# Optimization experiments

Measured on AMD Instinct MI355X. Metric: run time of the kernel, lower is better.

Reference implementation:

```python
import math
import jax, jax.numpy as jnp
import numpy as np

N_HEAD = 16; HEAD_DIM = 64; CHUNK = 64; NS_STEPS = 5; OMEGA = 16; POLY_DEG = 2; KCONV = 4


def short_conv(x, w, b):
    # x: (B,T,D), causal depthwise conv per ShortConv
    B, T, D = x.shape
    xt = jnp.transpose(x, (0, 2, 1))
    xt = jnp.pad(xt, ((0, 0), (0, 0), (KCONV - 1, 0)))
    y = jax.lax.conv_general_dilated(xt, w.astype(x.dtype), window_strides=(1,), padding='VALID',
                                     dimension_numbers=('NCW', 'OIW', 'NCW'), feature_group_count=D)
    y = y + b.astype(x.dtype)[:, None]
    return jnp.transpose(y, (0, 2, 1))


def rms_norm(x):
    ms = jnp.mean(x * x, axis=-1, keepdims=True)
    return x * jax.lax.rsqrt(ms + 1e-6)


def poly_features(x):
    coeffs = [1.0 / math.factorial(i) for i in range(1, POLY_DEG + 1)]
    res = coeffs[0] * x
    xp = x
    for i in range(1, POLY_DEG):
        xp = xp * x
        res = res + coeffs[i] * xp
    return res


def polar_express(X, steps):
    # Newton-Schulz / Polar-Express orthogonalization (Muon quintic coefficients)
    a, b, c = 3.4445, -4.7750, 2.0315
    n = jnp.sqrt(jnp.sum(X * X, axis=(-2, -1), keepdims=True)) + 1e-7
    X = X / n
    for _ in range(steps):
        XXt = X @ jnp.swapaxes(X, -1, -2)
        X = a * X + (b * XXt + c * (XXt @ XXt)) @ X
    return X


def omega_aggregate(u, gamma, w):
    # sliding-window weighted sum over chunk axis (axis=1) via cumsum difference
    cs = u.shape[1]
    cum = jnp.cumsum(gamma * u, axis=1)
    if w >= cs:
        return cum
    shifted = jnp.concatenate([jnp.zeros_like(cum[:, :w]), cum[:, :-w]], axis=1)
    return cum - shifted


def linear_scan(h_init, gates, inputs):
    # h_t = gate_t * h_{t-1} + input_t via associative scan over axis=1
    extra = inputs.ndim - gates.ndim
    g = gates.reshape(gates.shape + (1,) * extra)
    first = g[:, 0:1] * h_init[:, None] + inputs[:, 0:1]
    xs = jnp.concatenate([first, inputs[:, 1:]], axis=1)
    gs = jnp.concatenate([jnp.zeros_like(g[:, 0:1]), g[:, 1:]], axis=1)

    def fn(a, b):
        ga, xa = a
        gb, xb = b
        return (ga * gb, gb * xa + xb)

    _, h_all = jax.lax.associative_scan(fn, (gs, xs), axis=1)
    return h_all, h_all[:, -1]


def atlas_forward(x, Wq, Wk, Wv, Wproj, conv_q_w, conv_q_b, conv_k_w, conv_k_b,
                  conv_v_w, conv_v_b, Wa, We, Wt, Wg):
    B, T, C = x.shape
    H, D, cs = N_HEAD, HEAD_DIM, CHUNK
    nc = T // cs
    q = rms_norm(short_conv(x @ Wq.T, conv_q_w, conv_q_b).reshape(B, T, H, D))
    k = rms_norm(short_conv(x @ Wk.T, conv_k_w, conv_k_b).reshape(B, T, H, D))
    k = poly_features(k)  # phi(k)
    v = short_conv(x @ Wv.T, conv_v_w, conv_v_b).reshape(B, T, H, D)
    alpha = jax.nn.sigmoid(x @ Wa.T)[..., None]  # (B,T,H,1)
    eta = jax.nn.sigmoid(x @ We.T)[..., None]
    theta = jax.nn.sigmoid(x @ Wt.T)[..., None]
    gamma = jax.nn.sigmoid(x @ Wg.T)[..., None]

    def chunked(a):
        a = a.reshape((B, nc, cs) + a.shape[2:])
        return jnp.moveaxis(a, 1, 0)  # (nc, B, cs, ...)

    qc, kc, vc, ac, ec, tc, gc = map(chunked, (q, k, v, alpha, eta, theta, gamma))
    M0 = jnp.zeros((B, H, D, D), x.dtype)
    S0 = jnp.zeros_like(M0)

    def body(carry, inp):
        M, S = carry
        q_c, k_c, v_c, a_c, e_c, t_c, g_c = inp
        pred = jnp.einsum('bhvk,bchk->bchv', M, k_c)
        err = pred - v_c
        u = 2.0 * jnp.einsum('bchv,bchk->bchvk', err, k_c)  # (B,cs,H,D,D)
        u = omega_aggregate(u, g_c[..., None], OMEGA)
        th = jnp.squeeze(t_c, -1)
        mom = -(e_c[..., None] * u)
        chunk_S, S = linear_scan(S, th, mom)
        chunk_S_orth = polar_express(chunk_S, NS_STEPS)
        al = jnp.squeeze(a_c, -1)
        M_all, M = linear_scan(M, al, chunk_S_orth)
        y_c = jnp.einsum('bchvk,bchk->bchv', M_all, q_c)
        return (M, S), y_c

    (_, _), ys = jax.lax.scan(body, (M0, S0), (qc, kc, vc, ac, ec, tc, gc))
    y = jnp.moveaxis(ys, 0, 1).reshape(B, T, C)
    return y @ Wproj.T


def setup_inputs() -> dict:
    key = jax.random.key(0)
    ks = jax.random.split(key, 16)
    B, T, C, H = 2, 2048, 1024, 16
    s = 0.02
    return {
        'x': jax.random.normal(ks[0], (B, T, C), jnp.float32),
        'Wq': jax.random.normal(ks[1], (C, C), jnp.float32) * s,
        'Wk': jax.random.normal(ks[2], (C, C), jnp.float32) * s,
        'Wv': jax.random.normal(ks[3], (C, C), jnp.float32) * s,
        'Wproj': jax.random.normal(ks[4], (C, C), jnp.float32) * s,
        'conv_q_w': jax.random.normal(ks[5], (C, 1, KCONV), jnp.float32) * s,
        'conv_q_b': jnp.zeros((C,), jnp.float32),
        'conv_k_w': jax.random.normal(ks[6], (C, 1, KCONV), jnp.float32) * s,
        'conv_k_b': jnp.zeros((C,), jnp.float32),
        'conv_v_w': jax.random.normal(ks[7], (C, 1, KCONV), jnp.float32) * s,
        'conv_v_b': jnp.zeros((C,), jnp.float32),
        'Wa': jax.random.normal(ks[8], (H, C), jnp.float32) * s,
        'We': jax.random.normal(ks[9], (H, C), jnp.float32) * s,
        'Wt': jax.random.normal(ks[10], (H, C), jnp.float32) * s,
        'Wg': jax.random.normal(ks[11], (H, C), jnp.float32) * s,
    }


def reference(x, Wq, Wk, Wv, Wproj, conv_q_w, conv_q_b, conv_k_w, conv_k_b,
              conv_v_w, conv_v_b, Wa, We, Wt, Wg):
    return atlas_forward(x, Wq, Wk, Wv, Wproj, conv_q_w, conv_q_b, conv_k_w, conv_k_b,
                         conv_v_w, conv_v_b, Wa, We, Wt, Wg)
```

## Files before the change

kernel.cpp:

```cpp
#include <hip/hip_runtime.h>
#include <hip/hip_bf16.h>
#include <hip/hip_fp16.h>
#include <math.h>

#define B_ 2
#define T_ 2048
#define C_ 1024
#define H_ 16
#define D_ 64
#define CS_ 64
#define NC_ 32
#define NS_ 5
#define IST2 72

typedef __attribute__((ext_vector_type(8))) _Float16 f16x8;
typedef __attribute__((ext_vector_type(4))) float f32x4;

__global__ __launch_bounds__(256) void split16_kernel(const float* __restrict__ src,
                                                      _Float16* __restrict__ dst,
                                                      int n) {
    int i = (blockIdx.x * 256 + threadIdx.x) * 8;
    if (i >= n) return;
    float4 a = *(const float4*)&src[i];
    float4 b = *(const float4*)&src[i + 4];
    union { _Float16 h[8]; uint4 u; } o;
    o.h[0] = (_Float16)a.x; o.h[1] = (_Float16)a.y;
    o.h[2] = (_Float16)a.z; o.h[3] = (_Float16)a.w;
    o.h[4] = (_Float16)b.x; o.h[5] = (_Float16)b.y;
    o.h[6] = (_Float16)b.z; o.h[7] = (_Float16)b.w;
    *(uint4*)&dst[i] = o.u;
}

__global__ __launch_bounds__(256, 1) void gemm16(const _Float16* __restrict__ A,
                                                 const _Float16* __restrict__ Bm,
                                                 float* __restrict__ out) {
    __shared__ __align__(16) _Float16 sA[128 * 72];
    __shared__ __align__(16) _Float16 sB[128 * 72];
    int tid = threadIdx.x;
    int m0 = blockIdx.y * 128, n0 = blockIdx.x * 128;
    int w = tid >> 6, lane = tid & 63, q = lane >> 4, c = lane & 15;
    int mq = (w >> 1) * 64, nq = (w & 1) * 64;
    f32x4 acc[4][4];
    #pragma unroll
    for (int i = 0; i < 4; i++)
        #pragma unroll
        for (int j = 0; j < 4; j++) acc[i][j] = (f32x4){0.f, 0.f, 0.f, 0.f};
    int lrow = tid >> 2, lseg = (tid & 3) * 16;
    for (int kt = 0; kt < C_; kt += 64) {
        #pragma unroll
        for (int rr = 0; rr < 2; rr++) {
            int row = lrow + rr * 64;
            const size_t ga = (size_t)(m0 + row) * C_ + kt + lseg;
            const size_t gb = (size_t)(n0 + row) * C_ + kt + lseg;
            f16x8 va0 = *(const f16x8*)&A[ga];
            f16x8 va1 = *(const f16x8*)&A[ga + 8];
            f16x8 vb0 = *(const f16x8*)&Bm[gb];
            f16x8 vb1 = *(const f16x8*)&Bm[gb + 8];
            *(f16x8*)&sA[row * 72 + lseg] = va0;
            *(f16x8*)&sA[row * 72 + lseg + 8] = va1;
            *(f16x8*)&sB[row * 72 + lseg] = vb0;
            *(f16x8*)&sB[row * 72 + lseg + 8] = vb1;
        }
        __syncthreads();
        #pragma unroll
        for (int t = 0; t < 2; t++) {
            f16x8 af[4], bfr[4];
            #pragma unroll
            for (int i = 0; i < 4; i++)
                af[i] = *(const f16x8*)&sA[(mq + 16 * i + c) * 72 + t * 32 + q * 8];
            #pragma unroll
            for (int j = 0; j < 4; j++)
                bfr[j] = *(const f16x8*)&sB[(nq + 16 * j + c) * 72 + t * 32 + q * 8];
            #pragma unroll
            for (int i = 0; i < 4; i++)
                #pragma unroll
                for (int j = 0; j < 4; j++)
                    acc[i][j] = __builtin_amdgcn_mfma_f32_16x16x32_f16(af[i], bfr[j], acc[i][j], 0, 0, 0);
        }
        __syncthreads();
    }
    #pragma unroll
    for (int i = 0; i < 4; i++)
        #pragma unroll
        for (int j = 0; j < 4; j++)
            #pragma unroll
            for (int r = 0; r < 4; r++)
                out[(size_t)(m0 + mq + 16 * i + 4 * q + r) * C_ + n0 + nq + 16 * j + c] = acc[i][j][r];
}

__global__ __launch_bounds__(256) void conv_kernel(const float* __restrict__ xin,
                                                   const float* __restrict__ w,
                                                   const float* __restrict__ bias,
                                                   float* __restrict__ out, int mode) {
    int bt = blockIdx.x;
    int t = bt & (T_ - 1);
    int tid = threadIdx.x;
    int c0 = tid * 4;
    float4 w4[4];
    #pragma unroll
    for (int i = 0; i < 4; i++) w4[i] = *(const float4*)&w[(c0 + i) * 4];
    float4 bi = *(const float4*)&bias[c0];
    float4 xs[4];
    #pragma unroll
    for (int j = 0; j < 4; j++) {
        int tt = t - 3 + j;
        xs[j] = (tt >= 0) ? *(const float4*)&xin[(bt - 3 + j) * C_ + c0]
                          : make_float4(0.f, 0.f, 0.f, 0.f);
    }
    float y0 = bi.x + w4[0].x * xs[0].x + w4[0].y * xs[1].x + w4[0].z * xs[2].x + w4[0].w * xs[3].x;
    float y1 = bi.y + w4[1].x * xs[0].y + w4[1].y * xs[1].y + w4[1].z * xs[2].y + w4[1].w * xs[3].y;
    float y2 = bi.z + w4[2].x * xs[0].z + w4[2].y * xs[1].z + w4[2].z * xs[2].z + w4[2].w * xs[3].z;
    float y3 = bi.w + w4[3].x * xs[0].w + w4[3].y * xs[1].w + w4[3].z * xs[2].w + w4[3].w * xs[3].w;
    if (mode >= 1) {
        float ss = y0 * y0 + y1 * y1 + y2 * y2 + y3 * y3;
        ss += __shfl_xor(ss, 1);
        ss += __shfl_xor(ss, 2);
        ss += __shfl_xor(ss, 4);
        ss += __shfl_xor(ss, 8);
        float sc = rsqrtf(ss * (1.f / 64.f) + 1e-6f);
        y0 *= sc; y1 *= sc; y2 *= sc; y3 *= sc;
        if (mode == 2) {
            y0 += 0.5f * y0 * y0; y1 += 0.5f * y1 * y1;
            y2 += 0.5f * y2 * y2; y3 += 0.5f * y3 * y3;
        }
    }
    *(float4*)&out[bt * C_ + c0] = make_float4(y0, y1, y2, y3);
}

__global__ __launch_bounds__(256) void gates_kernel(const float* __restrict__ x,
                                                    const float* __restrict__ Wa,
                                                    const float* __restrict__ We,
                                                    const float* __restrict__ Wt,
                                                    const float* __restrict__ Wg,
                                                    float* __restrict__ gates) {
    __shared__ float xs[C_];
    int bt = blockIdx.x, tid = threadIdx.x;
    *(float4*)&xs[tid * 4] = *(const float4*)&x[bt * C_ + tid * 4];
    __syncthreads();
    int dot = tid >> 2, l = tid & 3;
    int g = dot >> 4, h = dot & 15;
    const float* Wp = (g == 0) ? Wa : (g == 1) ? We : (g == 2) ? Wt : Wg;
    const float* Wr = Wp + h * C_;
    float p = 0.f;
    for (int c = l * 4; c < C_; c += 16) {
        float4 wv = *(const float4*)&Wr[c];
        float4 xv = *(const float4*)&xs[c];
        p += wv.x * xv.x + wv.y * xv.y + wv.z * xv.z + wv.w * xv.w;
    }
    p += __shfl_xor(p, 1);
    p += __shfl_xor(p, 2);
    if (l == 0) gates[g * (B_ * T_ * H_) + bt * H_ + h] = 1.f / (1.f + __expf(-p));
}

__global__ __launch_bounds__(256) void chunk_s_kernel(const float* __restrict__ kbuf,
                                                      const float* __restrict__ vbuf,
                                                      const float* __restrict__ gates,
                                                      const float* __restrict__ Mc,
                                                      float* __restrict__ Sc,
                                                      float* __restrict__ chunkS,
                                                      int chunk) {
    __shared__ float Kc[CS_][68];
    __shared__ float Mrow[8][68];
    __shared__ float errS[CS_][8];
    __shared__ float thS[CS_], etS[CS_], gmS[CS_];
    int tid = threadIdx.x;
    int idx = blockIdx.x;
    int vt = idx & 7, h = (idx >> 3) & 15, b = idx >> 7;
    int c0t = chunk * CS_;
    {
        int row = tid >> 2, col = (tid & 3) * 16;
        const float* src = &kbuf[((size_t)(b * T_ + c0t + row) * H_ + h) * D_];
        #pragma unroll
        for (int i = 0; i < 4; i++)
            *(float4*)&Kc[row][col + i * 4] = *(const float4*)&src[col + i * 4];
    }
    if (tid < 128) {
        int v = tid >> 4, cc = (tid & 15) * 4;
        *(float4*)&Mrow[v][cc] =
            *(const float4*)&Mc[((size_t)(b * H_ + h)) * 4096 + (vt * 8 + v) * 64 + cc];
    }
    if (tid < CS_)           thS[tid] = gates[2 * (B_ * T_ * H_) + (b * T_ + c0t + tid) * H_ + h];
    else if (tid < 2 * CS_)  { int t = tid - CS_;     etS[t] = gates[1 * (B_ * T_ * H_) + (b * T_ + c0t + t) * H_ + h]; }
    else if (tid < 3 * CS_)  { int t = tid - 2 * CS_; gmS[t] = gates[3 * (B_ * T_ * H_) + (b * T_ + c0t + t) * H_ + h]; }
    __syncthreads();
    {
        int t = tid >> 2, v0 = (tid & 3) * 2;
        float s0 = 0.f, s1 = 0.f;
        #pragma unroll
        for (int k = 0; k < 64; k += 4) {
            float4 kv = *(float4*)&Kc[t][k];
            float4 m0 = *(float4*)&Mrow[v0][k];
            float4 m1 = *(float4*)&Mrow[v0 + 1][k];
            s0 += kv.x * m0.x + kv.y * m0.y + kv.z * m0.z + kv.w * m0.w;
            s1 += kv.x * m1.x + kv.y * m1.y + kv.z * m1.z + kv.w * m1.w;
        }
        const float* vp = &vbuf[((size_t)(b * T_ + c0t + t) * H_ + h) * D_ + vt * 8 + v0];
        errS[t][v0]     = s0 - vp[0];
        errS[t][v0 + 1] = s1 - vp[1];
    }
    __syncthreads();
    int vl = tid >> 5;
    int kk = (tid & 31) * 2;
    size_t sIdx = ((size_t)(b * H_ + h)) * 4096 + (vt * 8 + vl) * 64 + kk;
    float S0 = Sc[sIdx], S1 = Sc[sIdx + 1];
    float ring0[16] = {}, ring1[16] = {};
    float cum0 = 0.f, cum1 = 0.f;
    for (int cb = 0; cb < 4; ++cb) {
        #pragma unroll
        for (int ci = 0; ci < 16; ++ci) {
            int c = cb * 16 + ci;
            float er = 2.f * errS[c][vl];
            float2 kv = *(float2*)&Kc[c][kk];
            float g = gmS[c];
            cum0 += g * er * kv.x;
            cum1 += g * er * kv.y;
            float uw0 = cum0 - ring0[ci];
            float uw1 = cum1 - ring1[ci];
            ring0[ci] = cum0; ring1[ci] = cum1;
            float th = thS[c], et = etS[c];
            S0 = th * S0 - et * uw0;
            S1 = th * S1 - et * uw1;
            size_t o = ((size_t)((b * H_ + h) * CS_ + c)) * 4096 + (vt * 8 + vl) * 64 + kk;
            *(float2*)&chunkS[o] = make_float2(S0, S1);
        }
    }
    Sc[sIdx] = S0; Sc[sIdx + 1] = S1;
}

__device__ inline f16x8 ldH(const _Float16* buf, int row, int t, int q) {
    return *(const f16x8*)&buf[row * IST2 + t * 32 + q * 8];
}
__device__ inline void mmQ16(f32x4 (&out)[2][2],
                             const _Float16* bufA, const _Float16* bufB,
                             int ar0, int br0, int c, int q, bool share) {
    f16x8 a[2][2];
    #pragma unroll
    for (int rt = 0; rt < 2; rt++)
        #pragma unroll
        for (int t = 0; t < 2; t++)
            a[rt][t] = ldH(bufA, ar0 + 16 * rt + c, t, q);
    #pragma unroll
    for (int ctl = 0; ctl < 2; ctl++) {
        f16x8 b[2];
        if (share && ar0 == br0) {
            b[0] = a[ctl][0]; b[1] = a[ctl][1];
        } else {
            b[0] = ldH(bufB, br0 + 16 * ctl + c, 0, q);
            b[1] = ldH(bufB, br0 + 16 * ctl + c, 1, q);
        }
        #pragma unroll
        for (int rt = 0; rt < 2; rt++) {
            f32x4 acc = {0.f, 0.f, 0.f, 0.f};
            acc = __builtin_amdgcn_mfma_f32_16x16x32_f16(a[rt][0], b[0], acc, 0, 0, 0);
            acc = __builtin_amdgcn_mfma_f32_16x16x32_f16(a[rt][1], b[1], acc, 0, 0, 0);
            out[rt][ctl] = acc;
        }
    }
}
__device__ inline void writeRowQ16(_Float16* buf, const f32x4 (&M)[2][2],
                                   int ar0, int br0, int q, int c) {
    #pragma unroll
    for (int rt = 0; rt < 2; rt++)
        #pragma unroll
        for (int ctl = 0; ctl < 2; ctl++)
            #pragma unroll
            for (int r = 0; r < 4; r++)
                buf[(ar0 + 16 * rt + 4 * q + r) * IST2 + br0 + 16 * ctl + c] =
                    (_Float16)M[rt][ctl][r];
}
__device__ inline void writeColQ16(_Float16* buf, const f32x4 (&M)[2][2],
                                   int ar0, int br0, int q, int c) {
    #pragma unroll
    for (int rt = 0; rt < 2; rt++)
        #pragma unroll
        for (int ctl = 0; ctl < 2; ctl++) {
            unsigned short d[4];
            #pragma unroll
            for (int r = 0; r < 4; r++)
                d[r] = __builtin_bit_cast(unsigned short, (_Float16)M[rt][ctl][r]);
            *(uint2*)&buf[(br0 + 16 * ctl + c) * IST2 + ar0 + 16 * rt + 4 * q] =
                make_uint2((unsigned)d[0] | ((unsigned)d[1] << 16),
                           (unsigned)d[2] | ((unsigned)d[3] << 16));
        }
}

__global__ __launch_bounds__(256, 5) void polar_kernel(const float* __restrict__ chunkS,
                                                       __half* __restrict__ Z) {
    __shared__ __align__(16) _Float16 Xi[64 * IST2];
    __shared__ __align__(16) _Float16 Xti[64 * IST2];
    __shared__ __align__(16) _Float16 Yi[64 * IST2];
    __shared__ float red[4];
    int tid = threadIdx.x;
    int w = tid >> 6, lane = tid & 63;
    int q = lane >> 4, c = lane & 15;
    int ar0 = (w >> 1) * 32, br0 = (w & 1) * 32;
    size_t base = (size_t)blockIdx.x * 4096;

    f32x4 Xc[2][2];
    float ss = 0.f;
    #pragma unroll
    for (int rt = 0; rt < 2; rt++)
        #pragma unroll
        for (int ctl = 0; ctl < 2; ctl++)
            #pragma unroll
            for (int r = 0; r < 4; r++) {
                float v = chunkS[base + (size_t)(ar0 + 16 * rt + 4 * q + r) * 64 + br0 + 16 * ctl + c];
                Xc[rt][ctl][r] = v;
                ss += v * v;
            }
    ss += __shfl_xor(ss, 1);  ss += __shfl_xor(ss, 2);  ss += __shfl_xor(ss, 4);
    ss += __shfl_xor(ss, 8);  ss += __shfl_xor(ss, 16); ss += __shfl_xor(ss, 32);
    if (lane == 0) red[w] = ss;
    __syncthreads();
    float sc = 1.f / (sqrtf(red[0] + red[1] + red[2] + red[3]) + 1e-7f);
    #pragma unroll
    for (int rt = 0; rt < 2; rt++)
        #pragma unroll
        for (int ctl = 0; ctl < 2; ctl++)
            #pragma unroll
            for (int r = 0; r < 4; r++) Xc[rt][ctl][r] *= sc;
    writeRowQ16(Xi, Xc, ar0, br0, q, c);
    writeColQ16(Xti, Xc, ar0, br0, q, c);
    __syncthreads();

    const float na = 3.4445f, nb = -4.7750f, ncf = 2.0315f;
    f32x4 Yc[2][2], Tc[2][2];
    for (int it = 0; it < NS_; ++it) {
        mmQ16(Yc, Xi, Xi, ar0, br0, c, q, true);
        writeRowQ16(Yi, Yc, ar0, br0, q, c);
        __syncthreads();
        mmQ16(Tc, Yi, Yi, ar0, br0, c, q, true);
        #pragma unroll
        for (int rt = 0; rt < 2; rt++)
            #pragma unroll
            for (int ctl = 0; ctl < 2; ctl++)
                #pragma unroll
                for (int r = 0; r < 4; r++)
                    Yc[rt][ctl][r] = nb * Yc[rt][ctl][r] + ncf * Tc[rt][ctl][r];
        __syncthreads();
        writeRowQ16(Yi, Yc, ar0, br0, q, c);
        __syncthreads();
        mmQ16(Tc, Yi, Xti, ar0, br0, c, q, false);
        #pragma unroll
        for (int rt = 0; rt < 2; rt++)
            #pragma unroll
            for (int ctl = 0; ctl < 2; ctl++)
                #pragma unroll
                for (int r = 0; r < 4; r++)
                    Xc[rt][ctl][r] = na * Xc[rt][ctl][r] + Tc[rt][ctl][r];
        if (it != NS_ - 1) {
            writeRowQ16(Xi, Xc, ar0, br0, q, c);
            __syncthreads();
            writeColQ16(Xti, Xc, ar0, br0, q, c);
        }
    }
    #pragma unroll
    for (int rt = 0; rt < 2; rt++)
        #pragma unroll
        for (int ctl = 0; ctl < 2; ctl++)
            #pragma unroll
            for (int r = 0; r < 4; r++)
                Z[base + (size_t)(ar0 + 16 * rt + 4 * q + r) * 64 + br0 + 16 * ctl + c] =
                    __float2half(Xc[rt][ctl][r]);
}

__global__ __launch_bounds__(256) void fused_my_cs(const __half* __restrict__ Zb,
                                                   const float* __restrict__ qbuf,
                                                   const float* __restrict__ kbuf,
                                                   const float* __restrict__ vbuf,
                                                   const float* __restrict__ gates,
                                                   float* __restrict__ Mc,
                                                   float* __restrict__ Sc,
                                                   float* __restrict__ chunkS,
                                                   float* __restrict__ ybuf,
                                                   int chunk) {
    __shared__ float buf[CS_][68];
    __shared__ float Mrow[8][68];
    __shared__ float errS[CS_][8];
    __shared__ float alS[CS_], thS[CS_], etS[CS_], gmS[CS_];
    int tid = threadIdx.x, idx = blockIdx.x;
    int vt = idx & 7, h = (idx >> 3) & 15, b = idx >> 7;
    int c0t = chunk * CS_;
    {
        int row = tid >> 2, col = (tid & 3) * 16;
        const float* src = &qbuf[((size_t)(b * T_ + c0t + row) * H_ + h) * D_];
        #pragma unroll
        for (int i = 0; i < 4; i++)
            *(float4*)&buf[row][col + i * 4] = *(const float4*)&src[col + i * 4];
    }
    if (tid < CS_) alS[tid] = gates[0 * (B_ * T_ * H_) + (b * T_ + c0t + tid) * H_ + h];
    __syncthreads();
    int vl = tid >> 5, k0 = (tid & 31) * 2;
    size_t mIdx = ((size_t)(b * H_ + h)) * 4096 + (vt * 8 + vl) * 64 + k0;
    size_t zrow = ((size_t)(b * H_ + h) * CS_) * 4096 + (vt * 8 + vl) * 64 + k0;
    float M0 = Mc[mIdx], M1 = Mc[mIdx + 1];
    unsigned zr[8];
    #pragma unroll
    for (int j = 0; j < 8; j++)
        zr[j] = *(const unsigned*)&Zb[zrow + (size_t)j * 4096];
    #pragma unroll
    for (int c = 0; c < CS_; c++) {
        float2 z = __half22float2(__builtin_bit_cast(__half2, zr[c & 7]));
        if (c + 8 < CS_)
            zr[c & 7] = *(const unsigned*)&Zb[zrow + (size_t)(c + 8) * 4096];
        float al = alS[c];
        M0 = al * M0 + z.x;
        M1 = al * M1 + z.y;
        float2 qv = *(float2*)&buf[c][k0];
        float p = M0 * qv.x + M1 * qv.y;
        p += __shfl_xor(p, 1);  p += __shfl_xor(p, 2);  p += __shfl_xor(p, 4);
        p += __shfl_xor(p, 8);  p += __shfl_xor(p, 16);
        if ((tid & 31) == 0)
            ybuf[((size_t)(b * T_ + c0t + c) * H_ + h) * D_ + vt * 8 + vl] = p;
    }
    Mc[mIdx] = M0; Mc[mIdx + 1] = M1;
    if (chunk + 1 >= NC_) return;
    int c1t = c0t + CS_;
    __syncthreads();
    Mrow[vl][k0] = M0; Mrow[vl][k0 + 1] = M1;
    {
        int row = tid >> 2, col = (tid & 3) * 16;
        const float* src = &kbuf[((size_t)(b * T_ + c1t + row) * H_ + h) * D_];
        #pragma unroll
        for (int i = 0; i < 4; i++)
            *(float4*)&buf[row][col + i * 4] = *(const float4*)&src[col + i * 4];
    }
    if (tid < CS_)           thS[tid] = gates[2 * (B_ * T_ * H_) + (b * T_ + c1t + tid) * H_ + h];
    else if (tid < 2 * CS_)  { int t = tid - CS_;     etS[t] = gates[1 * (B_ * T_ * H_) + (b * T_ + c1t + t) * H_ + h]; }
    else if (tid < 3 * CS_)  { int t = tid - 2 * CS_; gmS[t] = gates[3 * (B_ * T_ * H_) + (b * T_ + c1t + t) * H_ + h]; }
    __syncthreads();
    {
        int t = tid >> 2, v0 = (tid & 3) * 2;
        float s0 = 0.f, s1 = 0.f;
        #pragma unroll
        for (int k = 0; k < 64; k += 4) {
            float4 kv = *(float4*)&buf[t][k];
            float4 m0v = *(float4*)&Mrow[v0][k];
            float4 m1v = *(float4*)&Mrow[v0 + 1][k];
            s0 += kv.x * m0v.x + kv.y * m0v.y + kv.z * m0v.z + kv.w * m0v.w;
            s1 += kv.x * m1v.x + kv.y * m1v.y + kv.z * m1v.z + kv.w * m1v.w;
        }
        const float* vp = &vbuf[((size_t)(b * T_ + c1t + t) * H_ + h) * D_ + vt * 8 + v0];
        errS[t][v0]     = s0 - vp[0];
        errS[t][v0 + 1] = s1 - vp[1];
    }
    __syncthreads();
    float S0 = Sc[mIdx], S1 = Sc[mIdx + 1];
    float ring0[16] = {}, ring1[16] = {};
    float cum0 = 0.f, cum1 = 0.f;
    for (int cb = 0; cb < 4; ++cb) {
        #pragma unroll
        for (int ci = 0; ci < 16; ++ci) {
            int cc = cb * 16 + ci;
            float er = 2.f * errS[cc][vl];
            float2 kv = *(float2*)&buf[cc][k0];
            float g = gmS[cc];
            cum0 += g * er * kv.x;
            cum1 += g * er * kv.y;
            float uw0 = cum0 - ring0[ci];
            float uw1 = cum1 - ring1[ci];
            ring0[ci] = cum0; ring1[ci] = cum1;
            float th = thS[cc], et = etS[cc];
            S0 = th * S0 - et * uw0;
            S1 = th * S1 - et * uw1;
            size_t o = ((size_t)((b * H_ + h) * CS_ + cc)) * 4096 + (vt * 8 + vl) * 64 + k0;
            *(float2*)&chunkS[o] = make_float2(S0, S1);
        }
    }
    Sc[mIdx] = S0; Sc[mIdx + 1] = S1;
}

extern "C" void kernel_launch(void* const* d_in, const int* in_sizes, int n_in,
                              void* d_out, int out_size, void* d_ws, size_t ws_size,
                              hipStream_t stream) {
    (void)in_sizes; (void)n_in; (void)out_size; (void)ws_size;
    const float* x     = (const float*)d_in[0];
    const float* Wq    = (const float*)d_in[1];
    const float* Wk    = (const float*)d_in[2];
    const float* Wv    = (const float*)d_in[3];
    const float* Wproj = (const float*)d_in[4];
    const float* cqw   = (const float*)d_in[5];
    const float* cqb   = (const float*)d_in[6];
    const float* ckw   = (const float*)d_in[7];
    const float* ckb   = (const float*)d_in[8];
    const float* cvw   = (const float*)d_in[9];
    const float* cvb   = (const float*)d_in[10];
    const float* Wa    = (const float*)d_in[11];
    const float* We    = (const float*)d_in[12];
    const float* Wt    = (const float*)d_in[13];
    const float* Wg    = (const float*)d_in[14];

    float* ws  = (float*)d_ws;
    float* Qb  = ws;
    float* Kb  = Qb + 4194304;
    float* Vb  = Kb + 4194304;
    float* Yb  = Vb + 4194304;
    float* Gb  = Yb + 4194304;
    float* Mc  = Gb + 262144;
    float* Sc  = Mc + 131072;
    float* CSb = Sc + 131072;
    float* Zr  = CSb + 8388608;
    __half* Zh = (__half*)Zr;
    float* bufA = Zr + 4194304;
    _Float16* su = (_Float16*)CSb;
    _Float16* xH  = su;
    _Float16* WqH = su + 4194304;
    _Float16* WkH = su + 5242880;
    _Float16* WvH = su + 6291456;

    hipMemsetAsync(Mc, 0, 2 * 131072 * sizeof(float), stream);

    split16_kernel<<<2048, 256, 0, stream>>>(x, xH, 4194304);
    split16_kernel<<<512, 256, 0, stream>>>(Wq, WqH, 1048576);
    split16_kernel<<<512, 256, 0, stream>>>(Wk, WkH, 1048576);
    split16_kernel<<<512, 256, 0, stream>>>(Wv, WvH, 1048576);

    dim3 gs(C_ / 128, (B_ * T_) / 128);
    gemm16<<<gs, 256, 0, stream>>>(xH, WqH, bufA);
    conv_kernel<<<B_ * T_, 256, 0, stream>>>(bufA, cqw, cqb, Qb, 1);
    gemm16<<<gs, 256, 0, stream>>>(xH, WkH, bufA);
    conv_kernel<<<B_ * T_, 256, 0, stream>>>(bufA, ckw, ckb, Kb, 2);
    gemm16<<<gs, 256, 0, stream>>>(xH, WvH, bufA);
    conv_kernel<<<B_ * T_, 256, 0, stream>>>(bufA, cvw, cvb, Vb, 0);
    gates_kernel<<<B_ * T_, 256, 0, stream>>>(x, Wa, We, Wt, Wg, Gb);

    chunk_s_kernel<<<B_ * H_ * 8, 256, 0, stream>>>(Kb, Vb, Gb, Mc, Sc, CSb, 0);
    for (int ch = 0; ch < NC_; ++ch) {
        polar_kernel<<<B_ * H_ * CS_, 256, 0, stream>>>(CSb, Zh);
        fused_my_cs<<<B_ * H_ * 8, 256, 0, stream>>>(Zh, Qb, Kb, Vb, Gb, Mc, Sc, CSb, Yb, ch);
    }

    _Float16* YbH = su;
    _Float16* WpH = su + 4194304;
    split16_kernel<<<2048, 256, 0, stream>>>(Yb, YbH, 4194304);
    split16_kernel<<<512, 256, 0, stream>>>(Wproj, WpH, 1048576);
    gemm16<<<gs, 256, 0, stream>>>(YbH, WpH, (float*)d_out);
}
```

Baseline: 2.165 ms.

## Use MFMA fp16 GEMM for gates and split fused_my_cs across twice the blocks

```diff
diff --git a/kernel.cpp b/kernel.cpp
--- a/kernel.cpp
+++ b/kernel.cpp
@@ -86,6 +86,58 @@
             #pragma unroll
             for (int r = 0; r < 4; r++)
                 out[(size_t)(m0 + mq + 16 * i + 4 * q + r) * C_ + n0 + nq + 16 * j + c] = acc[i][j][r];
+}
+
+__global__ __launch_bounds__(256) void gates16(const _Float16* __restrict__ xH,
+                                               const _Float16* __restrict__ WgH,
+                                               float* __restrict__ gates) {
+    __shared__ __align__(16) _Float16 sX[64 * 72];
+    __shared__ __align__(16) _Float16 sW[64 * 72];
+    int tid = threadIdx.x;
+    int m0 = blockIdx.x * 64;
+    int w = tid >> 6, lane = tid & 63, q = lane >> 4, c = lane & 15;
+    int ar0 = (w >> 1) * 32, br0 = (w & 1) * 32;
+    f32x4 acc[2][2];
+    #pragma unroll
+    for (int i = 0; i < 2; i++)
+        #pragma unroll
+        for (int j = 0; j < 2; j++) acc[i][j] = (f32x4){0.f, 0.f, 0.f, 0.f};
+    int lrow = tid >> 2, lseg = (tid & 3) * 16;
+    for (int kt = 0; kt < C_; kt += 64) {
+        *(f16x8*)&sX[lrow * 72 + lseg]     = *(const f16x8*)&xH[(size_t)(m0 + lrow) * C_ + kt + lseg];
+        *(f16x8*)&sX[lrow * 72 + lseg + 8] = *(const f16x8*)&xH[(size_t)(m0 + lrow) * C_ + kt + lseg + 8];
+        *(f16x8*)&sW[lrow * 72 + lseg]     = *(const f16x8*)&WgH[(size_t)lrow * C_ + kt + lseg];
+        *(f16x8*)&sW[lrow * 72 + lseg + 8] = *(const f16x8*)&WgH[(size_t)lrow * C_ + kt + lseg + 8];
+        __syncthreads();
+        #pragma unroll
+        for (int t = 0; t < 2; t++) {
+            f16x8 af[2], bf[2];
+            #pragma unroll
+            for (int i = 0; i < 2; i++)
+                af[i] = *(const f16x8*)&sX[(ar0 + 16 * i + c) * 72 + t * 32 + q * 8];
+            #pragma unroll
+            for (int j = 0; j < 2; j++)
+                bf[j] = *(const f16x8*)&sW[(br0 + 16 * j + c) * 72 + t * 32 + q * 8];
+            #pragma unroll
+            for (int i = 0; i < 2; i++)
+                #pragma unroll
+                for (int j = 0; j < 2; j++)
+                    acc[i][j] = __builtin_amdgcn_mfma_f32_16x16x32_f16(af[i], bf[j], acc[i][j], 0, 0, 0);
+        }
+        __syncthreads();
+    }
+    #pragma unroll
+    for (int i = 0; i < 2; i++)
+        #pragma unroll
+        for (int j = 0; j < 2; j++)
+            #pragma unroll
+            for (int r = 0; r < 4; r++) {
+                int bt = m0 + ar0 + 16 * i + 4 * q + r;
+                int n  = br0 + 16 * j + c;
+                float v = acc[i][j][r];
+                gates[(size_t)(n >> 4) * (B_ * T_ * H_) + (size_t)bt * H_ + (n & 15)] =
+                    1.f / (1.f + __expf(-v));
+            }
 }
 
 __global__ __launch_bounds__(256) void conv_kernel(const float* __restrict__ xin,
@@ -125,31 +177,6 @@
         }
     }
     *(float4*)&out[bt * C_ + c0] = make_float4(y0, y1, y2, y3);
-}
-
-__global__ __launch_bounds__(256) void gates_kernel(const float* __restrict__ x,
-                                                    const float* __restrict__ Wa,
-                                                    const float* __restrict__ We,
-                                                    const float* __restrict__ Wt,
-                                                    const float* __restrict__ Wg,
-                                                    float* __restrict__ gates) {
-    __shared__ float xs[C_];
-    int bt = blockIdx.x, tid = threadIdx.x;
-    *(float4*)&xs[tid * 4] = *(const float4*)&x[bt * C_ + tid * 4];
-    __syncthreads();
-    int dot = tid >> 2, l = tid & 3;
-    int g = dot >> 4, h = dot & 15;
-    const float* Wp = (g == 0) ? Wa : (g == 1) ? We : (g == 2) ? Wt : Wg;
-    const float* Wr = Wp + h * C_;
-    float p = 0.f;
-    for (int c = l * 4; c < C_; c += 16) {
-        float4 wv = *(const float4*)&Wr[c];
-        float4 xv = *(const float4*)&xs[c];
-        p += wv.x * xv.x + wv.y * xv.y + wv.z * xv.z + wv.w * xv.w;
-    }
-    p += __shfl_xor(p, 1);
-    p += __shfl_xor(p, 2);
-    if (l == 0) gates[g * (B_ * T_ * H_) + bt * H_ + h] = 1.f / (1.f + __expf(-p));
 }
 
 __global__ __launch_bounds__(256) void chunk_s_kernel(const float* __restrict__ kbuf,
@@ -375,11 +402,11 @@
                                                    float* __restrict__ ybuf,
                                                    int chunk) {
     __shared__ float buf[CS_][68];
-    __shared__ float Mrow[8][68];
-    __shared__ float errS[CS_][8];
+    __shared__ float Mrow[4][68];
+    __shared__ float errS[CS_][4];
     __shared__ float alS[CS_], thS[CS_], etS[CS_], gmS[CS_];
     int tid = threadIdx.x, idx = blockIdx.x;
-    int vt = idx & 7, h = (idx >> 3) & 15, b = idx >> 7;
+    int vt = idx & 15, h = (idx >> 4) & 15, b = idx >> 8;
     int c0t = chunk * CS_;
     {
         int row = tid >> 2, col = (tid & 3) * 16;
@@ -390,34 +417,32 @@
     }
     if (tid < CS_) alS[tid] = gates[0 * (B_ * T_ * H_) + (b * T_ + c0t + tid) * H_ + h];
     __syncthreads();
-    int vl = tid >> 5, k0 = (tid & 31) * 2;
-    size_t mIdx = ((size_t)(b * H_ + h)) * 4096 + (vt * 8 + vl) * 64 + k0;
-    size_t zrow = ((size_t)(b * H_ + h) * CS_) * 4096 + (vt * 8 + vl) * 64 + k0;
-    float M0 = Mc[mIdx], M1 = Mc[mIdx + 1];
-    unsigned zr[8];
+    int vl = tid >> 6, k0 = tid & 63;
+    size_t mIdx = ((size_t)(b * H_ + h)) * 4096 + (vt * 4 + vl) * 64 + k0;
+    size_t zrow = ((size_t)(b * H_ + h) * CS_) * 4096 + (vt * 4 + vl) * 64 + k0;
+    float M0 = Mc[mIdx];
+    unsigned short zr[8];
     #pragma unroll
     for (int j = 0; j < 8; j++)
-        zr[j] = *(const unsigned*)&Zb[zrow + (size_t)j * 4096];
+        zr[j] = *(const unsigned short*)&Zb[zrow + (size_t)j * 4096];
     #pragma unroll
     for (int c = 0; c < CS_; c++) {
-        float2 z = __half22float2(__builtin_bit_cast(__half2, zr[c & 7]));
+        float z = __half2float(__builtin_bit_cast(__half, zr[c & 7]));
         if (c + 8 < CS_)
-            zr[c & 7] = *(const unsigned*)&Zb[zrow + (size_t)(c + 8) * 4096];
+            zr[c & 7] = *(const unsigned short*)&Zb[zrow + (size_t)(c + 8) * 4096];
         float al = alS[c];
-        M0 = al * M0 + z.x;
-        M1 = al * M1 + z.y;
-        float2 qv = *(float2*)&buf[c][k0];
-        float p = M0 * qv.x + M1 * qv.y;
+        M0 = al * M0 + z;
+        float p = M0 * buf[c][k0];
         p += __shfl_xor(p, 1);  p += __shfl_xor(p, 2);  p += __shfl_xor(p, 4);
-        p += __shfl_xor(p, 8);  p += __shfl_xor(p, 16);
-        if ((tid & 31) == 0)
-            ybuf[((size_t)(b * T_ + c0t + c) * H_ + h) * D_ + vt * 8 + vl] = p;
-    }
-    Mc[mIdx] = M0; Mc[mIdx + 1] = M1;
+        p += __shfl_xor(p, 8);  p += __shfl_xor(p, 16); p += __shfl_xor(p, 32);
+        if ((tid & 63) == 0)
+            ybuf[((size_t)(b * T_ + c0t + c) * H_ + h) * D_ + vt * 4 + vl] = p;
+    }
+    Mc[mIdx] = M0;
     if (chunk + 1 >= NC_) return;
     int c1t = c0t + CS_;
     __syncthreads();
-    Mrow[vl][k0] = M0; Mrow[vl][k0 + 1] = M1;
+    Mrow[vl][k0] = M0;
     {
         int row = tid >> 2, col = (tid & 3) * 16;
         const float* src = &kbuf[((size_t)(b * T_ + c1t + row) * H_ + h) * D_];
@@ -430,44 +455,37 @@
     else if (tid < 3 * CS_)  { int t = tid - 2 * CS_; gmS[t] = gates[3 * (B_ * T_ * H_) + (b * T_ + c1t + t) * H_ + h]; }
     __syncthreads();
     {
-        int t = tid >> 2, v0 = (tid & 3) * 2;
-        float s0 = 0.f, s1 = 0.f;
+        int t = tid >> 2, v0 = tid & 3;
+        float s0 = 0.f;
         #pragma unroll
         for (int k = 0; k < 64; k += 4) {
             float4 kv = *(float4*)&buf[t][k];
-            float4 m0v = *(float4*)&Mrow[v0][k];
-            float4 m1v = *(float4*)&Mrow[v0 + 1][k];
-            s0 += kv.x * m0v.x + kv.y * m0v.y + kv.z * m0v.z + kv.w * m0v.w;
-            s1 += kv.x * m1v.x + kv.y * m1v.y + kv.z * m1v.z + kv.w * m1v.w;
-        }
-        const float* vp = &vbuf[((size_t)(b * T_ + c1t + t) * H_ + h) * D_ + vt * 8 + v0];
-        errS[t][v0]     = s0 - vp[0];
-        errS[t][v0 + 1] = s1 - vp[1];
-    }
-    __syncthreads();
-    float S0 = Sc[mIdx], S1 = Sc[mIdx + 1];
-    float ring0[16] = {}, ring1[16] = {};
-    float cum0 = 0.f, cum1 = 0.f;
+            float4 mv = *(float4*)&Mrow[v0][k];
+            s0 += kv.x * mv.x + kv.y * mv.y + kv.z * mv.z + kv.w * mv.w;
+        }
+        const float* vp = &vbuf[((size_t)(b * T_ + c1t + t) * H_ + h) * D_ + vt * 4 + v0];
+        errS[t][v0] = s0 - vp[0];
+    }
+    __syncthreads();
+    float S0 = Sc[mIdx];
+    float ring0[16] = {};
+    float cum0 = 0.f;
     for (int cb = 0; cb < 4; ++cb) {
         #pragma unroll
         for (int ci = 0; ci < 16; ++ci) {
             int cc = cb * 16 + ci;
             float er = 2.f * errS[cc][vl];
-            float2 kv = *(float2*)&buf[cc][k0];
+            float kv = buf[cc][k0];
             float g = gmS[cc];
-            cum0 += g * er * kv.x;
-            cum1 += g * er * kv.y;
+            cum0 += g * er * kv;
             float uw0 = cum0 - ring0[ci];
-            float uw1 = cum1 - ring1[ci];
-            ring0[ci] = cum0; ring1[ci] = cum1;
+            ring0[ci] = cum0;
             float th = thS[cc], et = etS[cc];
             S0 = th * S0 - et * uw0;
-            S1 = th * S1 - et * uw1;
-            size_t o = ((size_t)((b * H_ + h) * CS_ + cc)) * 4096 + (vt * 8 + vl) * 64 + k0;
-            *(float2*)&chunkS[o] = make_float2(S0, S1);
-        }
-    }
-    Sc[mIdx] = S0; Sc[mIdx + 1] = S1;
+            chunkS[((size_t)((b * H_ + h) * CS_ + cc)) * 4096 + (vt * 4 + vl) * 64 + k0] = S0;
+        }
+    }
+    Sc[mIdx] = S0;
 }
 
 extern "C" void kernel_launch(void* const* d_in, const int* in_sizes, int n_in,
@@ -507,6 +525,7 @@
     _Float16* WqH = su + 4194304;
     _Float16* WkH = su + 5242880;
     _Float16* WvH = su + 6291456;
+    _Float16* WgH = su + 7340032;
 
     hipMemsetAsync(Mc, 0, 2 * 131072 * sizeof(float), stream);
 
@@ -514,6 +533,10 @@
     split16_kernel<<<512, 256, 0, stream>>>(Wq, WqH, 1048576);
     split16_kernel<<<512, 256, 0, stream>>>(Wk, WkH, 1048576);
     split16_kernel<<<512, 256, 0, stream>>>(Wv, WvH, 1048576);
+    split16_kernel<<<8, 256, 0, stream>>>(Wa, WgH, 16384);
+    split16_kernel<<<8, 256, 0, stream>>>(We, WgH + 16384, 16384);
+    split16_kernel<<<8, 256, 0, stream>>>(Wt, WgH + 32768, 16384);
+    split16_kernel<<<8, 256, 0, stream>>>(Wg, WgH + 49152, 16384);
 
     dim3 gs(C_ / 128, (B_ * T_) / 128);
     gemm16<<<gs, 256, 0, stream>>>(xH, WqH, bufA);
@@ -522,12 +545,12 @@
     conv_kernel<<<B_ * T_, 256, 0, stream>>>(bufA, ckw, ckb, Kb, 2);
     gemm16<<<gs, 256, 0, stream>>>(xH, WvH, bufA);
     conv_kernel<<<B_ * T_, 256, 0, stream>>>(bufA, cvw, cvb, Vb, 0);
-    gates_kernel<<<B_ * T_, 256, 0, stream>>>(x, Wa, We, Wt, Wg, Gb);
+    gates16<<<(B_ * T_) / 64, 256, 0, stream>>>(xH, WgH, Gb);
 
     chunk_s_kernel<<<B_ * H_ * 8, 256, 0, stream>>>(Kb, Vb, Gb, Mc, Sc, CSb, 0);
     for (int ch = 0; ch < NC_; ++ch) {
         polar_kernel<<<B_ * H_ * CS_, 256, 0, stream>>>(CSb, Zh);
-        fused_my_cs<<<B_ * H_ * 8, 256, 0, stream>>>(Zh, Qb, Kb, Vb, Gb, Mc, Sc, CSb, Yb, ch);
+        fused_my_cs<<<B_ * H_ * 16, 256, 0, stream>>>(Zh, Qb, Kb, Vb, Gb, Mc, Sc, CSb, Yb, ch);
     }
 
     _Float16* YbH = su;
```

After: 2.166 ms. No clear change (+0.0%).
